# Kernel tuning notes

Measured on AMD Instinct MI355X. Metric: run time of the kernel, lower is better.

The kernel has to match this reference:

```python
import jax, jax.numpy as jnp
import numpy as np

N_CELLS = 6
N_OPS = 5
HIDDEN = 1024
IN_DIM = 376
OUT_DIM = 17
MAX_OUTPUT = 1.0
TAU = 1.0
BATCH = 2048

# op order matches the torch module: Tanh, ReLU, ELU, LeakyReLU(0.01), NullOp
ACTS = [jnp.tanh, jax.nn.relu, jax.nn.elu,
        lambda v: jax.nn.leaky_relu(v, 0.01),
        lambda v: jnp.zeros_like(v)]


def _apply_ops(pre):
    # pre: [j, o, b, h] -> apply the o-th activation to the o-th slice
    return jnp.stack([ACTS[o](pre[:, o]) for o in range(N_OPS)], axis=1)


def setup_inputs() -> dict:
    key = jax.random.key(0)
    ks = jax.random.split(key, 8)
    bw0 = 1.0 / np.sqrt(IN_DIM)
    bwh = 1.0 / np.sqrt(HIDDEN)
    x = jax.random.normal(ks[0], (BATCH, IN_DIM), dtype=jnp.float32)
    # stacked edge weights: W0 for cell-0 edges (input_dim -> hidden),
    # Wh[i-1] for cell-i edges (hidden -> hidden), i = 1..n_cells-2
    W0 = jax.random.uniform(ks[1], (N_CELLS, N_OPS, IN_DIM, HIDDEN), minval=-bw0, maxval=bw0, dtype=jnp.float32)
    b0 = jax.random.uniform(ks[2], (N_CELLS, N_OPS, HIDDEN), minval=-bw0, maxval=bw0, dtype=jnp.float32)
    Wh = jax.random.uniform(ks[3], (N_CELLS - 2, N_CELLS, N_OPS, HIDDEN, HIDDEN), minval=-bwh, maxval=bwh, dtype=jnp.float32)
    bh = jax.random.uniform(ks[4], (N_CELLS - 2, N_CELLS, N_OPS, HIDDEN), minval=-bwh, maxval=bwh, dtype=jnp.float32)
    Wout = jax.random.uniform(ks[5], (HIDDEN, OUT_DIM), minval=-bwh, maxval=bwh, dtype=jnp.float32)
    bout = jax.random.uniform(ks[6], (OUT_DIM,), minval=-bwh, maxval=bwh, dtype=jnp.float32)
    log_alphas = jnp.full((N_CELLS - 1, N_CELLS, N_OPS), -np.log(N_OPS), dtype=jnp.float32)
    # Gumbel noise (the torch module draws this in self.sample())
    u = jax.random.uniform(ks[7], (N_CELLS - 1, N_CELLS, N_OPS), minval=1e-6, maxval=1.0 - 1e-6, dtype=jnp.float32)
    eps = -jnp.log(-jnp.log(u))
    return {"x": x, "W0": W0, "b0": b0, "Wh": Wh, "bh": bh,
            "Wout": Wout, "bout": bout, "log_alphas": log_alphas, "eps": eps}


def reference(x, W0, b0, Wh, bh, Wout, bout, log_alphas, eps):
    # Gumbel-softmax mixing weights over the op axis
    z = jax.nn.softmax((log_alphas + eps) / TAU, axis=-1)  # [n_cells-1, n_cells, n_ops]
    # cell 0 feeds every node j >= 1: one batched GEMM over (j, o)
    pre0 = jnp.einsum('bd,jodh->jobh', x, W0[1:]) + b0[1:, :, None, :]
    outs = [(1, _apply_ops(pre0))]  # (first absolute j index, [j, o, b, h])
    tmp = None
    for i in range(1, N_CELLS):
        # node i input: weighted sum over all incoming edges k < i and ops o
        acc = jnp.zeros((x.shape[0], HIDDEN), dtype=x.dtype)
        for k in range(i):
            start, arr = outs[k]
            acc = acc + jnp.einsum('o,obh->bh', z[k, i], arr[i - start])
        if i < N_CELLS - 1:
            # node i feeds nodes j > i: batched GEMM over (j, o)
            pre = jnp.einsum('bh,johg->jobg', acc, Wh[i - 1, i + 1:]) + bh[i - 1, i + 1:, :, None, :]
            outs.append((i + 1, _apply_ops(pre)))
        tmp = acc
    return MAX_OUTPUT * jnp.tanh(tmp @ Wout + bout)
```

## Files before the change

kernel.cpp:

```cpp
#include <hip/hip_runtime.h>
#include <hip/hip_fp16.h>

typedef unsigned short u16;
typedef _Float16 f16;
typedef __attribute__((ext_vector_type(4))) u16 u16x4;
typedef __attribute__((ext_vector_type(8))) f16 f16x8;
typedef __attribute__((ext_vector_type(4))) float f32x4;

#define BATCH   2048
#define IN_DIM  376
#define KPAD0   384
#define HIDDEN  1024
#define OUT_DIM 17

#define WS_Z    0
#define WS_X16  1024
#define WS_ACC  (WS_X16 + (size_t)BATCH*KPAD0*2)
#define WS_W0T  (WS_ACC + (size_t)5*BATCH*HIDDEN*2)
#define WS_WHT  (WS_W0T + (size_t)20*HIDDEN*KPAD0*2)

__device__ __constant__ int D_PREF[5] = {0, 0, 4, 7, 9};

__global__ void z_kernel(const float* __restrict__ la, const float* __restrict__ ep,
                         float* __restrict__ z) {
    int t = threadIdx.x;
    if (t >= 30) return;
    float v[5]; float mx = -1e30f;
    #pragma unroll
    for (int o = 0; o < 5; ++o) { v[o] = la[t*5+o] + ep[t*5+o]; mx = fmaxf(mx, v[o]); }
    float s = 0.f;
    #pragma unroll
    for (int o = 0; o < 5; ++o) { v[o] = expf(v[o] - mx); s += v[o]; }
    float inv = 1.f / s;
    #pragma unroll
    for (int o = 0; o < 5; ++o) z[t*5+o] = v[o] * inv;
}

__global__ void xcvt_kernel(const float* __restrict__ x, u16* __restrict__ x16) {
    int idx = blockIdx.x * 256 + threadIdx.x;
    int b = idx / KPAD0, c = idx % KPAD0;
    float v = (c < IN_DIM) ? x[(size_t)b*IN_DIM + c] : 0.f;
    f16 h = (f16)v;
    x16[idx] = __builtin_bit_cast(u16, h);
}

__global__ void wtrans0_kernel(const float* __restrict__ W0, u16* __restrict__ dst) {
    __shared__ u16 sT[64*68];
    int bid = blockIdx.x;
    int mat = bid / 96, rem = bid % 96;
    int kt = rem / 16, nt = rem % 16;
    int i = mat / 4 + 1, o = mat % 4;
    const float* src = W0 + (size_t)(i*5 + o) * IN_DIM * HIDDEN;
    int t = threadIdx.x;
    #pragma unroll
    for (int p = 0; p < 16; ++p) {
        int e = p*256 + t;
        int kr = e >> 6, nc = e & 63;
        int k = kt*64 + kr;
        float v = (k < IN_DIM) ? src[(size_t)k*HIDDEN + nt*64 + nc] : 0.f;
        f16 h = (f16)v;
        sT[nc*68 + kr] = __builtin_bit_cast(u16, h);
    }
    __syncthreads();
    u16* d = dst + (size_t)mat * HIDDEN * KPAD0;
    #pragma unroll
    for (int p = 0; p < 4; ++p) {
        int c = p*256 + t;
        int nc = c >> 4, k4 = (c & 15) * 4;
        u16x4 v;
        #pragma unroll
        for (int j = 0; j < 4; ++j) v[j] = sT[nc*68 + k4 + j];
        *(u16x4*)&d[(size_t)(nt*64 + nc)*KPAD0 + kt*64 + k4] = v;
    }
}

__global__ void wtransH_kernel(const float* __restrict__ Wh, u16* __restrict__ dst) {
    const int SK[10] = {1,1,1,1,2,2,2,3,3,4};
    const int SI[10] = {2,3,4,5,3,4,5,4,5,5};
    __shared__ u16 sT[64*68];
    int bid = blockIdx.x;
    int mat = bid >> 8, rem = bid & 255;
    int kt = rem / 16, nt = rem % 16;
    int e = mat / 4, o = mat % 4;
    int k_src = SK[e], i_src = SI[e];
    const float* src = Wh + (size_t)(((k_src-1)*6 + i_src)*5 + o) * HIDDEN * HIDDEN;
    int t = threadIdx.x;
    #pragma unroll
    for (int p = 0; p < 16; ++p) {
        int ee = p*256 + t;
        int kr = ee >> 6, nc = ee & 63;
        float v = src[(size_t)(kt*64 + kr)*HIDDEN + nt*64 + nc];
        f16 h = (f16)v;
        sT[nc*68 + kr] = __builtin_bit_cast(u16, h);
    }
    __syncthreads();
    u16* d = dst + (size_t)mat * HIDDEN * HIDDEN;
    #pragma unroll
    for (int p = 0; p < 4; ++p) {
        int c = p*256 + t;
        int nc = c >> 4, k4 = (c & 15) * 4;
        u16x4 v;
        #pragma unroll
        for (int j = 0; j < 4; ++j) v[j] = sT[nc*68 + k4 + j];
        *(u16x4*)&d[(size_t)(nt*64 + nc)*HIDDEN + kt*64 + k4] = v;
    }
}

__global__ __launch_bounds__(256)
void step_kernel(int stepi,
                 const u16* __restrict__ x16, u16* __restrict__ accb,
                 const u16* __restrict__ w0t, const u16* __restrict__ wht,
                 const float* __restrict__ b0, const float* __restrict__ bh,
                 const float* __restrict__ zws) {
    __shared__ u16 sA[64*36];
    __shared__ u16 sB[4][64*36];
    const int t = threadIdx.x;
    const int lane = t & 63, wid = t >> 6;
    const int l15 = lane & 15, lk = lane >> 4;
    const int m0 = blockIdx.x * 64;
    const int n0 = blockIdx.y * 64;
    const int colw = n0 + wid*16 + l15;

    f32x4 run[4] = {};

    for (int k = 0; k < stepi; ++k) {
        const u16* Ap; int ldA, nks, ldW;
        const u16* Wt; const float* bias;
        if (k == 0) {
            Ap = x16; ldA = KPAD0; nks = KPAD0/32;
            Wt = w0t + (size_t)((stepi-1)*4) * HIDDEN * KPAD0; ldW = KPAD0;
            bias = b0 + (size_t)(stepi*5) * HIDDEN;
        } else {
            Ap = accb + (size_t)(k-1) * BATCH * HIDDEN; ldA = HIDDEN; nks = HIDDEN/32;
            int eidx = D_PREF[k] + (stepi - k - 1);
            Wt = wht + (size_t)(eidx*4) * HIDDEN * HIDDEN; ldW = HIDDEN;
            bias = bh + (size_t)(((k-1)*6 + stepi)*5) * HIDDEN;
        }
        const float* zp = zws + (k*6 + stepi)*5;

        f32x4 acc[4][4] = {};

        for (int kb = 0; kb < nks; ++kb) {
            const int koff = kb * 32;
            #pragma unroll
            for (int p = 0; p < 2; ++p) {
                int c = t + p*256;
                int row = c >> 3, c4 = (c & 7) * 4;
                u16x4 v = *(const u16x4*)&Ap[(size_t)(m0 + row)*ldA + koff + c4];
                *(u16x4*)&sA[row*36 + c4] = v;
            }
            {
                const u16* Wop = Wt + (size_t)wid * HIDDEN * ldW;
                #pragma unroll
                for (int p = 0; p < 8; ++p) {
                    int c = lane + p*64;
                    int row = c >> 3, c4 = (c & 7) * 4;
                    u16x4 v = *(const u16x4*)&Wop[(size_t)(n0 + row)*ldW + koff + c4];
                    *(u16x4*)&sB[wid][row*36 + c4] = v;
                }
            }
            __syncthreads();
            union FA { f16x8 v; u16x4 h[2]; };
            FA af[4];
            #pragma unroll
            for (int f = 0; f < 4; ++f) {
                int off = (f*16 + l15)*36 + lk*8;
                af[f].h[0] = *(const u16x4*)&sA[off];
                af[f].h[1] = *(const u16x4*)&sA[off + 4];
            }
            #pragma unroll
            for (int o = 0; o < 4; ++o) {
                FA bf;
                int off = (wid*16 + l15)*36 + lk*8;
                bf.h[0] = *(const u16x4*)&sB[o][off];
                bf.h[1] = *(const u16x4*)&sB[o][off + 4];
                #pragma unroll
                for (int f = 0; f < 4; ++f)
                    acc[f][o] = __builtin_amdgcn_mfma_f32_16x16x32_f16(af[f].v, bf.v, acc[f][o], 0, 0, 0);
            }
            __syncthreads();
        }
        #pragma unroll
        for (int o = 0; o < 4; ++o) {
            float zv = zp[o];
            float bv = bias[(size_t)o*HIDDEN + colw];
            #pragma unroll
            for (int f = 0; f < 4; ++f) {
                #pragma unroll
                for (int r = 0; r < 4; ++r) {
                    float pre = acc[f][o][r] + bv;
                    float a;
                    if      (o == 0) a = tanhf(pre);
                    else if (o == 1) a = fmaxf(pre, 0.f);
                    else if (o == 2) a = (pre > 0.f) ? pre : expm1f(pre);
                    else             a = (pre > 0.f) ? pre : 0.01f * pre;
                    run[f][r] += zv * a;
                }
            }
        }
    }
    u16* accout = accb + (size_t)(stepi-1) * BATCH * HIDDEN;
    const int rb = m0 + lk*4;
    #pragma unroll
    for (int f = 0; f < 4; ++f) {
        #pragma unroll
        for (int r = 0; r < 4; ++r) {
            f16 h = (f16)run[f][r];
            accout[(size_t)(rb + f*16 + r)*HIDDEN + colw] = __builtin_bit_cast(u16, h);
        }
    }
}

__global__ void out_kernel(const u16* __restrict__ acc5, const float* __restrict__ Wout,
                           const float* __restrict__ bout, float* __restrict__ out) {
    int t = threadIdx.x;
    int g = t & 15, rl = t >> 4;
    int row = blockIdx.x * 16 + rl;
    const f16* a = (const f16*)acc5 + (size_t)row * HIDDEN;
    float s[OUT_DIM] = {};
    for (int kk = 0; kk < HIDDEN/16; ++kk) {
        int kidx = kk*16 + g;
        float av = (float)a[kidx];
        const float* wr = Wout + (size_t)kidx * OUT_DIM;
        #pragma unroll
        for (int j = 0; j < OUT_DIM; ++j) s[j] += av * wr[j];
    }
    #pragma unroll
    for (int m = 1; m < 16; m <<= 1) {
        #pragma unroll
        for (int j = 0; j < OUT_DIM; ++j) s[j] += __shfl_xor(s[j], m, 64);
    }
    if (g == 0) {
        #pragma unroll
        for (int j = 0; j < OUT_DIM; ++j)
            out[(size_t)row*OUT_DIM + j] = tanhf(s[j] + bout[j]);
    }
}

extern "C" void kernel_launch(void* const* d_in, const int* in_sizes, int n_in,
                              void* d_out, int out_size, void* d_ws, size_t ws_size,
                              hipStream_t stream) {
    const float* x    = (const float*)d_in[0];
    const float* W0   = (const float*)d_in[1];
    const float* b0   = (const float*)d_in[2];
    const float* Wh   = (const float*)d_in[3];
    const float* bh   = (const float*)d_in[4];
    const float* Wout = (const float*)d_in[5];
    const float* bout = (const float*)d_in[6];
    const float* la   = (const float*)d_in[7];
    const float* eps  = (const float*)d_in[8];
    float* out = (float*)d_out;

    char* ws = (char*)d_ws;
    float* zws = (float*)(ws + WS_Z);
    u16* x16  = (u16*)(ws + WS_X16);
    u16* accb = (u16*)(ws + WS_ACC);
    u16* w0t  = (u16*)(ws + WS_W0T);
    u16* wht  = (u16*)(ws + WS_WHT);

    z_kernel<<<1, 32, 0, stream>>>(la, eps, zws);
    xcvt_kernel<<<(BATCH*KPAD0)/256, 256, 0, stream>>>(x, x16);
    wtrans0_kernel<<<1920, 256, 0, stream>>>(W0, w0t);
    wtransH_kernel<<<10240, 256, 0, stream>>>(Wh, wht);
    for (int i = 1; i <= 5; ++i)
        step_kernel<<<dim3(32, 16), 256, 0, stream>>>(i, x16, accb, w0t, wht, b0, bh, zws);
    out_kernel<<<BATCH/16, 256, 0, stream>>>(accb + (size_t)4*BATCH*HIDDEN, Wout, bout, out);
}
```

Baseline: 1.085 ms.

## Split incoming edges across grid z with atomic fp32 accumulation and LDS direct loads

Each step kernel now runs one block per (tile, incoming edge) along grid z instead of looping over edges serially inside a block. Partial results are combined with fp32 atomicAdd into a zeroed buffer, and a separate pass converts it to fp16 for the next step's GEMM input. The K loop switches to 64-wide tiles loaded with global_load_lds 16-byte transfers into an XOR-swizzled LDS layout. This exposes more parallelism in the early steps and cuts VGPR staging, at the cost of atomics, an extra zero pass, extra conversion kernels, and nondeterministic summation order.

```diff
diff --git a/kernel.cpp b/kernel.cpp
--- a/kernel.cpp
+++ b/kernel.cpp
@@ -13,13 +13,20 @@
 #define HIDDEN  1024
 #define OUT_DIM 17
 
-#define WS_Z    0
-#define WS_X16  1024
-#define WS_ACC  (WS_X16 + (size_t)BATCH*KPAD0*2)
-#define WS_W0T  (WS_ACC + (size_t)5*BATCH*HIDDEN*2)
-#define WS_WHT  (WS_W0T + (size_t)20*HIDDEN*KPAD0*2)
+#define WS_Z     0
+#define WS_X16   1024
+#define WS_ACC16 (WS_X16 + (size_t)BATCH*KPAD0*2)
+#define WS_ACCF  (WS_ACC16 + (size_t)4*BATCH*HIDDEN*2)
+#define WS_W0T   (WS_ACCF + (size_t)5*BATCH*HIDDEN*4)
+#define WS_WHT   (WS_W0T + (size_t)20*HIDDEN*KPAD0*2)
 
 __device__ __constant__ int D_PREF[5] = {0, 0, 4, 7, 9};
+
+__device__ inline void gll16(const void* g, void* l) {
+    __builtin_amdgcn_global_load_lds(
+        (const __attribute__((address_space(1))) unsigned int*)g,
+        (__attribute__((address_space(3))) unsigned int*)l, 16, 0, 0);
+}
 
 __global__ void z_kernel(const float* __restrict__ la, const float* __restrict__ ep,
                          float* __restrict__ z) {
@@ -82,8 +89,7 @@
     int mat = bid >> 8, rem = bid & 255;
     int kt = rem / 16, nt = rem % 16;
     int e = mat / 4, o = mat % 4;
-    int k_src = SK[e], i_src = SI[e];
-    const float* src = Wh + (size_t)(((k_src-1)*6 + i_src)*5 + o) * HIDDEN * HIDDEN;
+    const float* src = Wh + (size_t)(((SK[e]-1)*6 + SI[e])*5 + o) * HIDDEN * HIDDEN;
     int t = threadIdx.x;
     #pragma unroll
     for (int p = 0; p < 16; ++p) {
@@ -106,121 +112,135 @@
     }
 }
 
+__global__ void zero_kernel(float* __restrict__ p) {
+    int idx = blockIdx.x * 256 + threadIdx.x;
+    *(f32x4*)&p[(size_t)idx*4] = (f32x4){0.f, 0.f, 0.f, 0.f};
+}
+
+__global__ void cvt_kernel(const float* __restrict__ src, u16* __restrict__ dst) {
+    int idx = blockIdx.x * 256 + threadIdx.x;
+    f32x4 v = *(const f32x4*)&src[(size_t)idx*4];
+    u16x4 h;
+    #pragma unroll
+    for (int j = 0; j < 4; ++j) { f16 x = (f16)v[j]; h[j] = __builtin_bit_cast(u16, x); }
+    *(u16x4*)&dst[(size_t)idx*4] = h;
+}
+
 __global__ __launch_bounds__(256)
 void step_kernel(int stepi,
-                 const u16* __restrict__ x16, u16* __restrict__ accb,
+                 const u16* __restrict__ x16, const u16* __restrict__ acc16,
+                 float* __restrict__ accf,
                  const u16* __restrict__ w0t, const u16* __restrict__ wht,
                  const float* __restrict__ b0, const float* __restrict__ bh,
                  const float* __restrict__ zws) {
-    __shared__ u16 sA[64*36];
-    __shared__ u16 sB[4][64*36];
+    __shared__ alignas(16) u16 sA[64*64];
+    __shared__ alignas(16) u16 sB[4][64*64];
     const int t = threadIdx.x;
     const int lane = t & 63, wid = t >> 6;
     const int l15 = lane & 15, lk = lane >> 4;
     const int m0 = blockIdx.x * 64;
     const int n0 = blockIdx.y * 64;
-    const int colw = n0 + wid*16 + l15;
-
-    f32x4 run[4] = {};
-
-    for (int k = 0; k < stepi; ++k) {
-        const u16* Ap; int ldA, nks, ldW;
-        const u16* Wt; const float* bias;
-        if (k == 0) {
-            Ap = x16; ldA = KPAD0; nks = KPAD0/32;
-            Wt = w0t + (size_t)((stepi-1)*4) * HIDDEN * KPAD0; ldW = KPAD0;
-            bias = b0 + (size_t)(stepi*5) * HIDDEN;
-        } else {
-            Ap = accb + (size_t)(k-1) * BATCH * HIDDEN; ldA = HIDDEN; nks = HIDDEN/32;
-            int eidx = D_PREF[k] + (stepi - k - 1);
-            Wt = wht + (size_t)(eidx*4) * HIDDEN * HIDDEN; ldW = HIDDEN;
-            bias = bh + (size_t)(((k-1)*6 + stepi)*5) * HIDDEN;
-        }
-        const float* zp = zws + (k*6 + stepi)*5;
-
-        f32x4 acc[4][4] = {};
-
-        for (int kb = 0; kb < nks; ++kb) {
-            const int koff = kb * 32;
-            #pragma unroll
-            for (int p = 0; p < 2; ++p) {
-                int c = t + p*256;
-                int row = c >> 3, c4 = (c & 7) * 4;
-                u16x4 v = *(const u16x4*)&Ap[(size_t)(m0 + row)*ldA + koff + c4];
-                *(u16x4*)&sA[row*36 + c4] = v;
+    const int k = blockIdx.z;
+
+    const u16* Ap; int ldA, nks;
+    const u16* Wt; int ldW;
+    const float* bias;
+    if (k == 0) {
+        Ap = x16; ldA = KPAD0; nks = KPAD0/64;
+        Wt = w0t + (size_t)((stepi-1)*4) * HIDDEN * KPAD0; ldW = KPAD0;
+        bias = b0 + (size_t)(stepi*5) * HIDDEN;
+    } else {
+        Ap = acc16 + (size_t)(k-1) * BATCH * HIDDEN; ldA = HIDDEN; nks = HIDDEN/64;
+        int eidx = D_PREF[k] + (stepi - k - 1);
+        Wt = wht + (size_t)(eidx*4) * HIDDEN * HIDDEN; ldW = HIDDEN;
+        bias = bh + (size_t)(((k-1)*6 + stepi)*5) * HIDDEN;
+    }
+    const float* zp = zws + (k*6 + stepi)*5;
+
+    const int srow = lane >> 3;
+    const int sc   = (lane & 7) ^ srow;
+
+    const u16* aG0 = Ap + (size_t)(m0 + wid*16 + srow)     * ldA + sc*8;
+    const u16* aG1 = Ap + (size_t)(m0 + wid*16 + 8 + srow) * ldA + sc*8;
+    u16* aL0 = &sA[(wid*2)   * 512];
+    u16* aL1 = &sA[(wid*2+1) * 512];
+    const u16* Wop = Wt + (size_t)wid * HIDDEN * ldW;
+    const u16* bG[8];
+    #pragma unroll
+    for (int p = 0; p < 8; ++p)
+        bG[p] = Wop + (size_t)(n0 + p*8 + srow) * ldW + sc*8;
+    u16* bL = &sB[wid][0];
+
+    f32x4 acc[4][4] = {};
+
+    for (int kb = 0; kb < nks; ++kb) {
+        const int koff = kb * 64;
+        gll16(aG0 + koff, aL0);
+        gll16(aG1 + koff, aL1);
+        #pragma unroll
+        for (int p = 0; p < 8; ++p)
+            gll16(bG[p] + koff, bL + p*512);
+        __syncthreads();
+        #pragma unroll
+        for (int kc = 0; kc < 2; ++kc) {
+            f16x8 af[4], bf[4];
+            #pragma unroll
+            for (int f = 0; f < 4; ++f) {
+                int row = f*16 + l15;
+                int cc = (kc*4 + lk) ^ (row & 7);
+                af[f] = *(const f16x8*)&sA[row*64 + cc*8];
             }
-            {
-                const u16* Wop = Wt + (size_t)wid * HIDDEN * ldW;
-                #pragma unroll
-                for (int p = 0; p < 8; ++p) {
-                    int c = lane + p*64;
-                    int row = c >> 3, c4 = (c & 7) * 4;
-                    u16x4 v = *(const u16x4*)&Wop[(size_t)(n0 + row)*ldW + koff + c4];
-                    *(u16x4*)&sB[wid][row*36 + c4] = v;
-                }
+            #pragma unroll
+            for (int o = 0; o < 4; ++o) {
+                int row = wid*16 + l15;
+                int cc = (kc*4 + lk) ^ (row & 7);
+                bf[o] = *(const f16x8*)&sB[o][row*64 + cc*8];
             }
-            __syncthreads();
-            union FA { f16x8 v; u16x4 h[2]; };
-            FA af[4];
-            #pragma unroll
-            for (int f = 0; f < 4; ++f) {
-                int off = (f*16 + l15)*36 + lk*8;
-                af[f].h[0] = *(const u16x4*)&sA[off];
-                af[f].h[1] = *(const u16x4*)&sA[off + 4];
-            }
-            #pragma unroll
-            for (int o = 0; o < 4; ++o) {
-                FA bf;
-                int off = (wid*16 + l15)*36 + lk*8;
-                bf.h[0] = *(const u16x4*)&sB[o][off];
-                bf.h[1] = *(const u16x4*)&sB[o][off + 4];
+            #pragma unroll
+            for (int o = 0; o < 4; ++o)
                 #pragma unroll
                 for (int f = 0; f < 4; ++f)
-                    acc[f][o] = __builtin_amdgcn_mfma_f32_16x16x32_f16(af[f].v, bf.v, acc[f][o], 0, 0, 0);
+                    acc[f][o] = __builtin_amdgcn_mfma_f32_16x16x32_f16(af[f], bf[o], acc[f][o], 0, 0, 0);
+        }
+        __syncthreads();
+    }
+
+    const int colw = n0 + wid*16 + l15;
+    float outv[4][4] = {};
+    #pragma unroll
+    for (int o = 0; o < 4; ++o) {
+        float zv = zp[o];
+        float bv = bias[(size_t)o*HIDDEN + colw];
+        #pragma unroll
+        for (int f = 0; f < 4; ++f)
+            #pragma unroll
+            for (int r = 0; r < 4; ++r) {
+                float pre = acc[f][o][r] + bv;
+                float a;
+                if      (o == 0) a = tanhf(pre);
+                else if (o == 1) a = fmaxf(pre, 0.f);
+                else if (o == 2) a = (pre > 0.f) ? pre : expm1f(pre);
+                else             a = (pre > 0.f) ? pre : 0.01f * pre;
+                outv[f][r] += zv * a;
             }
-            __syncthreads();
-        }
-        #pragma unroll
-        for (int o = 0; o < 4; ++o) {
-            float zv = zp[o];
-            float bv = bias[(size_t)o*HIDDEN + colw];
-            #pragma unroll
-            for (int f = 0; f < 4; ++f) {
-                #pragma unroll
-                for (int r = 0; r < 4; ++r) {
-                    float pre = acc[f][o][r] + bv;
-                    float a;
-                    if      (o == 0) a = tanhf(pre);
-                    else if (o == 1) a = fmaxf(pre, 0.f);
-                    else if (o == 2) a = (pre > 0.f) ? pre : expm1f(pre);
-                    else             a = (pre > 0.f) ? pre : 0.01f * pre;
-                    run[f][r] += zv * a;
-                }
-            }
-        }
-    }
-    u16* accout = accb + (size_t)(stepi-1) * BATCH * HIDDEN;
-    const int rb = m0 + lk*4;
-    #pragma unroll
-    for (int f = 0; f < 4; ++f) {
-        #pragma unroll
-        for (int r = 0; r < 4; ++r) {
-            f16 h = (f16)run[f][r];
-            accout[(size_t)(rb + f*16 + r)*HIDDEN + colw] = __builtin_bit_cast(u16, h);
-        }
-    }
-}
-
-__global__ void out_kernel(const u16* __restrict__ acc5, const float* __restrict__ Wout,
+    }
+    #pragma unroll
+    for (int f = 0; f < 4; ++f)
+        #pragma unroll
+        for (int r = 0; r < 4; ++r)
+            atomicAdd(&accf[(size_t)(m0 + f*16 + lk*4 + r)*HIDDEN + colw], outv[f][r]);
+}
+
+__global__ void out_kernel(const float* __restrict__ acc5, const float* __restrict__ Wout,
                            const float* __restrict__ bout, float* __restrict__ out) {
     int t = threadIdx.x;
     int g = t & 15, rl = t >> 4;
     int row = blockIdx.x * 16 + rl;
-    const f16* a = (const f16*)acc5 + (size_t)row * HIDDEN;
+    const float* a = acc5 + (size_t)row * HIDDEN;
     float s[OUT_DIM] = {};
     for (int kk = 0; kk < HIDDEN/16; ++kk) {
         int kidx = kk*16 + g;
-        float av = (float)a[kidx];
+        float av = a[kidx];
         const float* wr = Wout + (size_t)kidx * OUT_DIM;
         #pragma unroll
         for (int j = 0; j < OUT_DIM; ++j) s[j] += av * wr[j];
@@ -252,17 +272,26 @@
     float* out = (float*)d_out;
 
     char* ws = (char*)d_ws;
-    float* zws = (float*)(ws + WS_Z);
-    u16* x16  = (u16*)(ws + WS_X16);
-    u16* accb = (u16*)(ws + WS_ACC);
-    u16* w0t  = (u16*)(ws + WS_W0T);
-    u16* wht  = (u16*)(ws + WS_WHT);
+    float* zws  = (float*)(ws + WS_Z);
+    u16* x16    = (u16*)(ws + WS_X16);
+    u16* acc16  = (u16*)(ws + WS_ACC16);
+    float* accf = (float*)(ws + WS_ACCF);
+    u16* w0t    = (u16*)(ws + WS_W0T);
+    u16* wht    = (u16*)(ws + WS_WHT);
 
     z_kernel<<<1, 32, 0, stream>>>(la, eps, zws);
     xcvt_kernel<<<(BATCH*KPAD0)/256, 256, 0, stream>>>(x, x16);
     wtrans0_kernel<<<1920, 256, 0, stream>>>(W0, w0t);
     wtransH_kernel<<<10240, 256, 0, stream>>>(Wh, wht);
-    for (int i = 1; i <= 5; ++i)
-        step_kernel<<<dim3(32, 16), 256, 0, stream>>>(i, x16, accb, w0t, wht, b0, bh, zws);
-    out_kernel<<<BATCH/16, 256, 0, stream>>>(accb + (size_t)4*BATCH*HIDDEN, Wout, bout, out);
-}
+    zero_kernel<<<(5*BATCH*HIDDEN)/(4*256), 256, 0, stream>>>(accf);
+
+    for (int i = 1; i <= 5; ++i) {
+        float* accf_i = accf + (size_t)(i-1)*BATCH*HIDDEN;
+        step_kernel<<<dim3(32, 16, i), 256, 0, stream>>>(
+            i, x16, acc16, accf_i, w0t, wht, b0, bh, zws);
+        if (i < 5)
+            cvt_kernel<<<(BATCH*HIDDEN)/(4*256), 256, 0, stream>>>(
+                accf_i, acc16 + (size_t)(i-1)*BATCH*HIDDEN);
+    }
+    out_kernel<<<BATCH/16, 256, 0, stream>>>(accf + (size_t)4*BATCH*HIDDEN, Wout, bout, out);
+}
```

New measurement: 1.045 ms. 1.04x faster.
